# Performance work log

Measured on AMD Instinct MI355X. Metric: run time of the kernel, lower is better.

## Reference

```python
import jax, jax.numpy as jnp
import numpy as np

EPS = 1e-8
NUM_HEADS = 8
SCALE = 25.0
SIM_THRESH = 0.75
BLOCK = 10  # per-frame proposal group size used by the zeroing mask


def _l2norm(x):
    return x / (jnp.linalg.norm(x, axis=-1, keepdims=True) + EPS)


def setup_inputs() -> dict:
    key = jax.random.key(0)
    ks = jax.random.split(key, 7)
    B, N, C = 1, 2000, 256
    H = NUM_HEADS
    x_cls = jax.random.normal(ks[0], (B, N, C), dtype=jnp.float32)
    x_reg = jax.random.normal(ks[1], (B, N, C), dtype=jnp.float32)
    cls_score = jax.random.uniform(ks[2], (N,), dtype=jnp.float32)
    fg_score = jax.random.uniform(ks[3], (N,), dtype=jnp.float32)
    coord_attn = jax.random.uniform(ks[4], (B, H, N, N), dtype=jnp.float32)
    W_qkv_cls = jax.random.normal(ks[5], (3 * C, C), dtype=jnp.float32) * 0.02
    W_qkv_reg = jax.random.normal(ks[6], (3 * C, C), dtype=jnp.float32) * 0.02
    return {"x_cls": x_cls, "x_reg": x_reg, "cls_score": cls_score,
            "fg_score": fg_score, "coord_attn": coord_attn,
            "W_qkv_cls": W_qkv_cls, "W_qkv_reg": W_qkv_reg}


def reference(x_cls, x_reg, cls_score, fg_score, coord_attn, W_qkv_cls, W_qkv_reg):
    B, N, C = x_cls.shape
    H = NUM_HEADS
    D = C // H

    def qkv(x, W):
        t = (x @ W.T).reshape(B, N, 3, H, D).transpose(2, 0, 3, 1, 4)  # [3,B,H,N,D]
        return t[0], t[1], t[2]

    q_cls, k_cls, v_cls = qkv(x_cls, W_qkv_cls)
    q_reg, k_reg, v_reg = qkv(x_reg, W_qkv_reg)

    q_cls, k_cls = _l2norm(q_cls), _l2norm(k_cls)
    q_reg, k_reg = _l2norm(q_reg), _l2norm(k_reg)
    v_cls_normed = _l2norm(v_cls)

    cs = cls_score.reshape(1, 1, 1, N)  # broadcast over [B,H,N,N]
    fs = fg_score.reshape(1, 1, 1, N)

    attn_cls_raw = jnp.einsum('bhnd,bhmd->bhnm', v_cls_normed, v_cls_normed)

    attn_cls = jax.nn.softmax(jnp.einsum('bhnd,bhmd->bhnm', q_cls, k_cls) * SCALE * cs, axis=-1)
    attn_reg = jax.nn.softmax(jnp.einsum('bhnd,bhmd->bhnm', q_reg, k_reg) * SCALE * fs, axis=-1)

    attn = (attn_reg + attn_cls) * 0.5 * coord_attn
    attn = jax.lax.stop_gradient(attn)  # original detaches before masking

    # block-diagonal zeroing: row j zeros cols [j//10*10, j//10*10+9), keep diagonal
    rows = jnp.arange(N)[:, None]
    cols = jnp.arange(N)[None, :]
    block_start = (rows // BLOCK) * BLOCK
    zero_mask = (cols >= block_start) & (cols < block_start + (BLOCK - 1)) & (cols != rows)
    attn = jnp.where(zero_mask, 0.0, attn)

    x = jnp.einsum('bhnm,bhmd->bhnd', attn, v_cls).transpose(0, 2, 1, 3).reshape(B, N, C)
    x_ori = v_cls.transpose(0, 2, 1, 3).reshape(B, N, C)
    x_cat = jnp.concatenate([x, x_ori], axis=-1)  # [B,N,2C]

    # ave=True branch
    sim_raw = jnp.sum(attn_cls_raw, axis=1)[0] / H          # [N,N]
    sim_mask = (sim_raw > SIM_THRESH).astype(x_cls.dtype)
    sim_attn = jnp.sum(attn, axis=1)[0] / H                 # [N,N]
    sim_round2 = jax.nn.softmax(sim_attn, axis=-1)
    sim_round2 = sim_mask * sim_round2 / (jnp.sum(sim_mask * sim_round2, axis=-1, keepdims=True) + EPS)
    return x_cat, sim_round2
```

## Files before the change

### kernel.cpp

```cpp
#include <hip/hip_runtime.h>
#include <math.h>

typedef _Float16 half8 __attribute__((ext_vector_type(8)));
typedef _Float16 half4 __attribute__((ext_vector_type(4)));
typedef _Float16 half2v __attribute__((ext_vector_type(2)));
typedef float f32x4 __attribute__((ext_vector_type(4)));

constexpr int N = 2000;
constexpr int NP = 2048;
constexpr int H = 8;
constexpr int D = 32;
constexpr float SCL = 25.0f;
constexpr float L2E = 1.4426950408889634f;
constexpr float FM2 = 25.0f * L2E;

#define MFMA16(a,b,c)  __builtin_amdgcn_mfma_f32_16x16x32_f16((a),(b),(c),0,0,0)
#define MFMA16K(a,b,c) __builtin_amdgcn_mfma_f32_16x16x16f16((a),(b),(c),0,0,0)

__device__ __forceinline__ float fexp2(float x) { return __builtin_amdgcn_exp2f(x); }


__global__ __launch_bounds__(256) void wconv_kernel(
    const float* __restrict__ Wc, const float* __restrict__ Wr,
    _Float16* __restrict__ Wch, _Float16* __restrict__ Wrh)
{
    const int i = blockIdx.x * 256 + threadIdx.x;
    Wch[i] = (_Float16)Wc[i];
    Wrh[i] = (_Float16)Wr[i];
}

__global__ __launch_bounds__(256) void qkv_kernel(
    const float* __restrict__ xc, const float* __restrict__ xr,
    const _Float16* __restrict__ Wch, const _Float16* __restrict__ Wrh,
    const float* __restrict__ clsScore, const float* __restrict__ fgScore,
    _Float16* __restrict__ Qch, _Float16* __restrict__ Kch,
    _Float16* __restrict__ Qrh, _Float16* __restrict__ Krh,
    _Float16* __restrict__ Vnh, _Float16* __restrict__ Vth,
    float* __restrict__ out)
{
    constexpr int XS = 264;
    __shared__ _Float16 xs[16 * XS];
    const int t = threadIdx.x;
    const int n0 = blockIdx.x * 16;
    const int by = blockIdx.y;
    const int which = (by < 3) ? by : (by - 3);
    const bool isCls = by < 3;
    const float* x = isCls ? xc : xr;
    const _Float16* Wh = isCls ? Wch : Wrh;

    #pragma unroll
    for (int it = 0; it < 4; ++it) {
        const int f = t + it * 256;
        const int row = f >> 6, c4 = f & 63;
        const float4 v = *(const float4*)(x + (size_t)(n0 + row) * 256 + c4 * 4);
        half4 hv; hv[0]=(_Float16)v.x; hv[1]=(_Float16)v.y; hv[2]=(_Float16)v.z; hv[3]=(_Float16)v.w;
        *(half4*)&xs[row * XS + c4 * 4] = hv;
    }
    __syncthreads();

    const int w = t >> 6, l = t & 63;
    const int lr = l & 15, lg = l >> 4;
    const int obase = which * 256 + w * 64;
    f32x4 acc[4] = {{0,0,0,0},{0,0,0,0},{0,0,0,0},{0,0,0,0}};
    for (int k0 = 0; k0 < 256; k0 += 32) {
        const half8 aX = *(const half8*)&xs[lr * XS + k0 + lg * 8];
        #pragma unroll
        for (int s = 0; s < 4; ++s) {
            const half8 bW = *(const half8*)(Wh + (size_t)(obase + s * 16 + lr) * 256 + k0 + lg * 8);
            acc[s] = MFMA16(aX, bW, acc[s]);
        }
    }
    f32x4 kscale = {1.f,1.f,1.f,1.f};
    if (which == 1) {
        const float* sp = isCls ? clsScore : fgScore;
        kscale = (SCL * L2E) * *(const f32x4*)(sp + n0 + lg*4);
    }
    #pragma unroll
    for (int p = 0; p < 2; ++p) {
        const int h = 2 * w + p;
        float ss[4];
        #pragma unroll
        for (int j = 0; j < 4; ++j) {
            float v = acc[2*p][j]*acc[2*p][j] + acc[2*p+1][j]*acc[2*p+1][j];
            #pragma unroll
            for (int off = 1; off < 16; off <<= 1) v += __shfl_xor(v, off);
            ss[j] = sqrtf(v) + 1e-8f;
        }
        if (which < 2) {
            _Float16* Qd = isCls ? (which == 0 ? Qch : Kch) : (which == 0 ? Qrh : Krh);
            #pragma unroll
            for (int sh = 0; sh < 2; ++sh)
                #pragma unroll
                for (int j = 0; j < 4; ++j)
                    Qd[((size_t)h*NP + n0 + lg*4 + j)*D + sh*16 + lr]
                        = (_Float16)(acc[2*p+sh][j] / ss[j] * kscale[j]);
        } else {
            #pragma unroll
            for (int sh = 0; sh < 2; ++sh) {
                const int d = sh * 16 + lr;
                half4 tv;
                #pragma unroll
                for (int j = 0; j < 4; ++j) {
                    const float raw = acc[2*p+sh][j];
                    Vnh[((size_t)h*NP + n0 + lg*4 + j)*D + d] = (_Float16)(raw / ss[j]);
                    out[(size_t)(n0 + lg*4 + j)*512 + 256 + h*D + d] = raw;
                    tv[j] = (_Float16)raw;
                }
                *(half4*)(Vth + ((size_t)h*D + d)*NP + n0 + lg*4) = tv;
            }
        }
    }
}

__global__ __launch_bounds__(512) void stats_kernel(
    const _Float16* __restrict__ Qch, const _Float16* __restrict__ Kch,
    const _Float16* __restrict__ Qrh, const _Float16* __restrict__ Krh,
    float* __restrict__ BIAS)
{
    __shared__ float Ssh[4][2][16];
    const int t = threadIdx.x;
    const int w = t >> 6, l = t & 63;
    const int nsub = w >> 1, mhalf = w & 1;
    const int n0 = blockIdx.x * 64 + nsub * 16;
    const int h = blockIdx.y, z = blockIdx.z;
    const _Float16* Q = z ? Qrh : Qch;
    const _Float16* K = z ? Krh : Kch;
    const int lr = l & 15, lg = l >> 4;
    const half8 aQ = *(const half8*)(Q + ((size_t)h*NP + n0 + lr)*D + lg*8);
    float S[4] = {0.f, 0.f, 0.f, 0.f};
    const int msBeg = mhalf ? 63 : 0;
    const int msEnd = mhalf ? 125 : 63;
    half8 bK = *(const half8*)(K + ((size_t)h*NP + msBeg*16 + lr)*D + lg*8);
    for (int ms = msBeg; ms < msEnd; ++ms) {
        const half8 cur = bK;
        if (ms + 1 < msEnd)
            bK = *(const half8*)(K + ((size_t)h*NP + (ms+1)*16 + lr)*D + lg*8);
        f32x4 z4 = {0.f, 0.f, 0.f, 0.f};
        const f32x4 c = MFMA16(aQ, cur, z4);
        #pragma unroll
        for (int j = 0; j < 4; ++j) S[j] += fexp2(c[j] - FM2);
    }
    #pragma unroll
    for (int j = 0; j < 4; ++j) {
        #pragma unroll
        for (int off = 1; off < 16; off <<= 1) S[j] += __shfl_xor(S[j], off);
    }
    if (lr == 0) {
        #pragma unroll
        for (int j = 0; j < 4; ++j) Ssh[nsub][mhalf][lg*4 + j] = S[j];
    }
    __syncthreads();
    if (t < 64) {
        const int ns = t >> 4, rl = t & 15;
        BIAS[((size_t)z*H + h)*NP + blockIdx.x*64 + ns*16 + rl]
            = -__log2f(Ssh[ns][0][rl] + Ssh[ns][1][rl]) - FM2 - 1.0f;
    }
}

__global__ __launch_bounds__(256) void vvmask_kernel(
    const _Float16* __restrict__ Vnh, unsigned char* __restrict__ Mask)
{
    const int t = threadIdx.x;
    const int w = t >> 6, l = t & 63;
    const int n0 = blockIdx.y * 16;
    const int m00 = blockIdx.x * 256 + w * 64;
    const int lr = l & 15, lg = l >> 4;
    half8 aV[8];
    #pragma unroll
    for (int h = 0; h < 8; ++h)
        aV[h] = *(const half8*)(Vnh + ((size_t)(h*NP + n0 + lr))*D + lg*8);
    for (int s = 0; s < 4; ++s) {
        const int mb = m00 + s*16;
        f32x4 acc = {0.f, 0.f, 0.f, 0.f};
        #pragma unroll
        for (int h = 0; h < 8; ++h) {
            const half8 bV = *(const half8*)(Vnh + ((size_t)(h*NP + mb + lr))*D + lg*8);
            acc = MFMA16(aV[h], bV, acc);
        }
        const int m = mb + lr;
        if (m < N) {
            #pragma unroll
            for (int j = 0; j < 4; ++j) {
                const int n = n0 + lg*4 + j;
                Mask[(size_t)n*N + m] = (acc[j]*0.125f > 0.75f) ? (unsigned char)1 : (unsigned char)0;
            }
        }
    }
}

template<int SMAX>
__global__ __launch_bounds__(256, 4) void attn_kernel(
    const _Float16* __restrict__ Kch, const _Float16* __restrict__ Krh,
    const _Float16* __restrict__ Qch, const _Float16* __restrict__ Qrh,
    const _Float16* __restrict__ Vth, const float* __restrict__ coord,
    const float* __restrict__ BIAS,
    _Float16* __restrict__ SIMH, _Float16* __restrict__ XPH, int mcBase)
{
    __shared__ _Float16 simred[4][16][136];

    const int t = threadIdx.x;
    const int w = t >> 6, l = t & 63;
    const int lr = l & 15, lg = l >> 4;
    const int mc = mcBase + blockIdx.x;
    const int m0 = mc * 128;
    const int n0 = blockIdx.y * 16;
    const int n = n0 + lr;
    const int bs = (n / 10) * 10;
    const int h0 = 2 * w;

    unsigned kill = 0u;
    #pragma unroll
    for (int s = 0; s < SMAX; ++s)
        #pragma unroll
        for (int j = 0; j < 4; ++j) {
            const int m = m0 + s*16 + lg*4 + j;
            if (m >= bs && m < bs + 9 && m != n) kill |= (1u << (s*4 + j));
        }

    half8 aQc[2], aQr[2]; float bC[2], bR[2];
    #pragma unroll
    for (int p = 0; p < 2; ++p) {
        const int h = h0 + p;
        aQc[p] = *(const half8*)(Qch + ((size_t)h*NP + n)*D + lg*8);
        aQr[p] = *(const half8*)(Qrh + ((size_t)h*NP + n)*D + lg*8);
        bC[p] = BIAS[(size_t)h*NP + n];
        bR[p] = BIAS[(size_t)(H + h)*NP + n];
    }

    half2v sacc[SMAX][2];
    #pragma unroll
    for (int s = 0; s < SMAX; ++s)
        #pragma unroll
        for (int k = 0; k < 2; ++k) { sacc[s][k][0] = (_Float16)0.f; sacc[s][k][1] = (_Float16)0.f; }

    half8 kc[2], kr[2]; half4 v0[2], v1[2]; f32x4 co[2];
    auto LOAD = [&](int it) {
        const int p = it / SMAX, s = it % SMAX, b = it & 1;
        const int h = h0 + p;
        const size_t kb = ((size_t)h*NP + m0 + s*16 + lr)*D + lg*8;
        kc[b] = *(const half8*)(Kch + kb);
        kr[b] = *(const half8*)(Krh + kb);
        v0[b] = *(const half4*)(Vth + ((size_t)(h*D + lr))*NP + m0 + s*16 + lg*4);
        v1[b] = *(const half4*)(Vth + ((size_t)(h*D + 16 + lr))*NP + m0 + s*16 + lg*4);
        co[b] = *(const f32x4*)(coord + ((size_t)h*N + n)*N + m0 + s*16 + lg*4);
    };

    f32x4 pv0 = {0,0,0,0}, pv1 = {0,0,0,0};
    LOAD(0);
    #pragma unroll
    for (int it = 0; it < 2*SMAX; ++it) {
        const int p = it / SMAX, s = it % SMAX, b = it & 1;
        if (it + 1 < 2*SMAX) LOAD(it + 1);
        f32x4 z4 = {0.f,0.f,0.f,0.f};
        const f32x4 cc = MFMA16(kc[b], aQc[p], z4);
        const f32x4 cr = MFMA16(kr[b], aQr[p], z4);
        half4 af;
        #pragma unroll
        for (int j = 0; j < 4; ++j) {
            float a = (fexp2(cc[j] + bC[p]) + fexp2(cr[j] + bR[p])) * co[b][j];
            if ((kill >> (s*4 + j)) & 1u) a = 0.f;
            af[j] = (_Float16)a;
        }
        sacc[s][0] += (half2v){af[0], af[1]};
        sacc[s][1] += (half2v){af[2], af[3]};
        pv0 = MFMA16K(af, v0[b], pv0);
        pv1 = MFMA16K(af, v1[b], pv1);
        if (s == SMAX - 1) {
            const int h = h0 + p;
            _Float16* xp = XPH + (((size_t)(mc*H + h)*N + n0 + lg*4))*D + lr;
            #pragma unroll
            for (int j = 0; j < 4; ++j) {
                xp[j*D]      = (_Float16)pv0[j];
                xp[j*D + 16] = (_Float16)pv1[j];
            }
            pv0 = (f32x4){0,0,0,0}; pv1 = (f32x4){0,0,0,0};
        }
    }

    #pragma unroll
    for (int s = 0; s < SMAX; ++s) {
        half4 sv; sv[0]=sacc[s][0][0]; sv[1]=sacc[s][0][1]; sv[2]=sacc[s][1][0]; sv[3]=sacc[s][1][1];
        *(half4*)&simred[w][lr][s*16 + lg*4] = sv;
    }
    __syncthreads();
    constexpr int C8 = SMAX * 2;
    for (int e = t; e < 16 * C8; e += 256) {
        const int r = e / C8, c8 = e % C8;
        const half8 s0 = *(const half8*)&simred[0][r][c8*8];
        const half8 s1 = *(const half8*)&simred[1][r][c8*8];
        const half8 s2 = *(const half8*)&simred[2][r][c8*8];
        const half8 s3 = *(const half8*)&simred[3][r][c8*8];
        const half8 sum = (s0 + s1) + (s2 + s3);
        *(half8*)(SIMH + (size_t)(n0 + r)*N + m0 + c8*8) = sum;
    }
}

__global__ __launch_bounds__(256) void reduce_kernel(
    const _Float16* __restrict__ XPH, float* __restrict__ out)
{
    const int n = blockIdx.x, t = threadIdx.x;
    const int h = t >> 5, d = t & 31;
    float acc = 0.f;
    #pragma unroll
    for (int mcI = 0; mcI < 16; ++mcI)
        acc += (float)XPH[(((size_t)mcI*H + h)*N + n)*D + d];
    out[(size_t)n*512 + t] = acc;
}

__global__ __launch_bounds__(256) void simfinal_kernel(
    const _Float16* __restrict__ SIMH, const unsigned char* __restrict__ Mask,
    float* __restrict__ out)
{
    __shared__ float redA[4], redB[4];
    const int n = blockIdx.x, t = threadIdx.x;
    const _Float16* row = SIMH + (size_t)n * N;
    const unsigned char* mrow = Mask + (size_t)n * N;
    const bool act = t < 250;
    float f[8];
    unsigned int mk0 = 0, mk1 = 0;
    float mx = -1e30f;
    if (act) {
        const half8 v8 = *(const half8*)(row + t*8);
        const uint2 mm = *(const uint2*)(mrow + t*8);
        mk0 = mm.x; mk1 = mm.y;
        #pragma unroll
        for (int k = 0; k < 8; ++k) { f[k] = (float)v8[k]; mx = fmaxf(mx, f[k]); }
    }
    #pragma unroll
    for (int off = 1; off < 64; off <<= 1) mx = fmaxf(mx, __shfl_xor(mx, off));
    const int wv = t >> 6;
    if ((t & 63) == 0) redA[wv] = mx;
    __syncthreads();
    const float M = fmaxf(fmaxf(redA[0], redA[1]), fmaxf(redA[2], redA[3]));
    float e[8];
    float sA = 0.f, sM = 0.f;
    if (act) {
        #pragma unroll
        for (int k = 0; k < 8; ++k) {
            e[k] = fexp2((f[k] - M) * (L2E * 0.125f));
            sA += e[k];
            const unsigned int mkb = ((k < 4 ? mk0 : mk1) >> (8*(k & 3))) & 0xffu;
            if (mkb) sM += e[k]; else e[k] = 0.f;
        }
    }
    #pragma unroll
    for (int off = 1; off < 64; off <<= 1) { sA += __shfl_xor(sA, off); sM += __shfl_xor(sM, off); }
    __syncthreads();
    if ((t & 63) == 0) { redA[wv] = sA; redB[wv] = sM; }
    __syncthreads();
    const float SA = redA[0] + redA[1] + redA[2] + redA[3];
    const float SMK = redB[0] + redB[1] + redB[2] + redB[3];
    const float inv = 1.f / (SMK + 1e-8f * SA);
    if (act) {
        float* orow = out + 1024000 + (size_t)n*N + t*8;
        *(float4*)(orow)     = make_float4(e[0]*inv, e[1]*inv, e[2]*inv, e[3]*inv);
        *(float4*)(orow + 4) = make_float4(e[4]*inv, e[5]*inv, e[6]*inv, e[7]*inv);
    }
}

extern "C" void kernel_launch(void* const* d_in, const int* in_sizes, int n_in,
                              void* d_out, int out_size, void* d_ws, size_t ws_size,
                              hipStream_t stream) {
    const float* x_cls     = (const float*)d_in[0];
    const float* x_reg     = (const float*)d_in[1];
    const float* cls_score = (const float*)d_in[2];
    const float* fg_score  = (const float*)d_in[3];
    const float* coord     = (const float*)d_in[4];
    const float* Wc        = (const float*)d_in[5];
    const float* Wr        = (const float*)d_in[6];

    char* base = (char*)d_ws;
    float* BIAS     = (float*)base;
    _Float16* SIMH  = (_Float16*)(base + 131072);
    _Float16* XPH   = (_Float16*)(base + 8131072);
    _Float16* Qch   = (_Float16*)(base + 24515072);
    _Float16* Kch   = Qch + 524288;
    _Float16* Qrh   = Qch + 2*524288;
    _Float16* Krh   = Qch + 3*524288;
    _Float16* Vnh   = Qch + 4*524288;
    _Float16* Vth   = Qch + 5*524288;
    _Float16* Wch   = (_Float16*)(base + 30806528);
    _Float16* Wrh   = (_Float16*)(base + 31199744);
    unsigned char* Mask = (unsigned char*)(base + 31592960);
    float* out = (float*)d_out;

    wconv_kernel<<<768, 256, 0, stream>>>(Wc, Wr, Wch, Wrh);
    qkv_kernel<<<dim3(125, 5), 256, 0, stream>>>(x_cls, x_reg, Wch, Wrh, cls_score, fg_score,
                                                 Qch, Kch, Qrh, Krh, Vnh, Vth, out);
    stats_kernel<<<dim3(32, 8, 2), 512, 0, stream>>>(Qch, Kch, Qrh, Krh, BIAS);
    vvmask_kernel<<<dim3(8, 125), 256, 0, stream>>>(Vnh, Mask);
    attn_kernel<8><<<dim3(15, 125), 256, 0, stream>>>(Kch, Krh, Qch, Qrh, Vth, coord,
                                                      BIAS, SIMH, XPH, 0);
    attn_kernel<5><<<dim3(1, 125), 256, 0, stream>>>(Kch, Krh, Qch, Qrh, Vth, coord,
                                                     BIAS, SIMH, XPH, 15);
    reduce_kernel<<<2000, 256, 0, stream>>>(XPH, out);
    simfinal_kernel<<<2000, 256, 0, stream>>>(SIMH, Mask, out);
}
```

Baseline: 144.2 us.

## Deepen coord prefetch, raise attn occupancy, split stats key range four ways

The attention kernel now loads the coord_attn tile two iterations ahead using a three-slot buffer, separate from the one-ahead K/V prefetch, and its launch bounds ask for 5 blocks per SM instead of 4. The stats kernel now handles 32 query rows per block and splits the key range across four waves instead of two, giving 63 blocks per head instead of 32. The aim is to hide the latency of the large coord stream and to fill the GPU better in stats. The catch is more register pressure, which may cause spills under the tighter occupancy target.

```diff
diff --git a/kernel.cpp b/kernel.cpp
--- a/kernel.cpp
+++ b/kernel.cpp
@@ -117,23 +117,23 @@
     const _Float16* __restrict__ Qrh, const _Float16* __restrict__ Krh,
     float* __restrict__ BIAS)
 {
-    __shared__ float Ssh[4][2][16];
+    __shared__ float Ssh[2][4][16];
     const int t = threadIdx.x;
     const int w = t >> 6, l = t & 63;
-    const int nsub = w >> 1, mhalf = w & 1;
-    const int n0 = blockIdx.x * 64 + nsub * 16;
+    const int nsub = w >> 2, mq = w & 3;
+    const int n0 = blockIdx.x * 32 + nsub * 16;
     const int h = blockIdx.y, z = blockIdx.z;
     const _Float16* Q = z ? Qrh : Qch;
     const _Float16* K = z ? Krh : Kch;
     const int lr = l & 15, lg = l >> 4;
     const half8 aQ = *(const half8*)(Q + ((size_t)h*NP + n0 + lr)*D + lg*8);
     float S[4] = {0.f, 0.f, 0.f, 0.f};
-    const int msBeg = mhalf ? 63 : 0;
-    const int msEnd = mhalf ? 125 : 63;
-    half8 bK = *(const half8*)(K + ((size_t)h*NP + msBeg*16 + lr)*D + lg*8);
-    for (int ms = msBeg; ms < msEnd; ++ms) {
+    const int mqB0 = (mq == 0) ? 0 : 31*mq;
+    const int mqB1 = (mq == 3) ? 125 : 31*(mq+1);
+    half8 bK = *(const half8*)(K + ((size_t)h*NP + mqB0*16 + lr)*D + lg*8);
+    for (int ms = mqB0; ms < mqB1; ++ms) {
         const half8 cur = bK;
-        if (ms + 1 < msEnd)
+        if (ms + 1 < mqB1)
             bK = *(const half8*)(K + ((size_t)h*NP + (ms+1)*16 + lr)*D + lg*8);
         f32x4 z4 = {0.f, 0.f, 0.f, 0.f};
         const f32x4 c = MFMA16(aQ, cur, z4);
@@ -147,13 +147,14 @@
     }
     if (lr == 0) {
         #pragma unroll
-        for (int j = 0; j < 4; ++j) Ssh[nsub][mhalf][lg*4 + j] = S[j];
-    }
-    __syncthreads();
-    if (t < 64) {
+        for (int j = 0; j < 4; ++j) Ssh[nsub][mq][lg*4 + j] = S[j];
+    }
+    __syncthreads();
+    if (t < 32) {
         const int ns = t >> 4, rl = t & 15;
-        BIAS[((size_t)z*H + h)*NP + blockIdx.x*64 + ns*16 + rl]
-            = -__log2f(Ssh[ns][0][rl] + Ssh[ns][1][rl]) - FM2 - 1.0f;
+        const int n = blockIdx.x * 32 + ns*16 + rl;
+        BIAS[((size_t)z*H + h)*NP + n]
+            = -__log2f(Ssh[ns][0][rl] + Ssh[ns][1][rl] + Ssh[ns][2][rl] + Ssh[ns][3][rl]) - FM2 - 1.0f;
     }
 }
 
@@ -189,7 +190,7 @@
 }
 
 template<int SMAX>
-__global__ __launch_bounds__(256, 4) void attn_kernel(
+__global__ __launch_bounds__(256, 5) void attn_kernel(
     const _Float16* __restrict__ Kch, const _Float16* __restrict__ Krh,
     const _Float16* __restrict__ Qch, const _Float16* __restrict__ Qrh,
     const _Float16* __restrict__ Vth, const float* __restrict__ coord,
@@ -233,8 +234,13 @@
         #pragma unroll
         for (int k = 0; k < 2; ++k) { sacc[s][k][0] = (_Float16)0.f; sacc[s][k][1] = (_Float16)0.f; }
 
-    half8 kc[2], kr[2]; half4 v0[2], v1[2]; f32x4 co[2];
-    auto LOAD = [&](int it) {
+    half8 kc[2], kr[2]; half4 v0[2], v1[2]; f32x4 co[3];
+    auto LOADCO = [&](int it) {
+        const int p = it / SMAX, s = it % SMAX, c = it % 3;
+        const int h = h0 + p;
+        co[c] = *(const f32x4*)(coord + ((size_t)h*N + n)*N + m0 + s*16 + lg*4);
+    };
+    auto LOADKV = [&](int it) {
         const int p = it / SMAX, s = it % SMAX, b = it & 1;
         const int h = h0 + p;
         const size_t kb = ((size_t)h*NP + m0 + s*16 + lr)*D + lg*8;
@@ -242,22 +248,24 @@
         kr[b] = *(const half8*)(Krh + kb);
         v0[b] = *(const half4*)(Vth + ((size_t)(h*D + lr))*NP + m0 + s*16 + lg*4);
         v1[b] = *(const half4*)(Vth + ((size_t)(h*D + 16 + lr))*NP + m0 + s*16 + lg*4);
-        co[b] = *(const f32x4*)(coord + ((size_t)h*N + n)*N + m0 + s*16 + lg*4);
     };
 
     f32x4 pv0 = {0,0,0,0}, pv1 = {0,0,0,0};
-    LOAD(0);
+    LOADCO(0);
+    if (2*SMAX > 1) LOADCO(1);
+    LOADKV(0);
     #pragma unroll
     for (int it = 0; it < 2*SMAX; ++it) {
-        const int p = it / SMAX, s = it % SMAX, b = it & 1;
-        if (it + 1 < 2*SMAX) LOAD(it + 1);
+        const int p = it / SMAX, s = it % SMAX, b = it & 1, c = it % 3;
+        if (it + 2 < 2*SMAX) LOADCO(it + 2);
+        if (it + 1 < 2*SMAX) LOADKV(it + 1);
         f32x4 z4 = {0.f,0.f,0.f,0.f};
         const f32x4 cc = MFMA16(kc[b], aQc[p], z4);
         const f32x4 cr = MFMA16(kr[b], aQr[p], z4);
         half4 af;
         #pragma unroll
         for (int j = 0; j < 4; ++j) {
-            float a = (fexp2(cc[j] + bC[p]) + fexp2(cr[j] + bR[p])) * co[b][j];
+            float a = (fexp2(cc[j] + bC[p]) + fexp2(cr[j] + bR[p])) * co[c][j];
             if ((kill >> (s*4 + j)) & 1u) a = 0.f;
             af[j] = (_Float16)a;
         }
@@ -387,7 +395,7 @@
     wconv_kernel<<<768, 256, 0, stream>>>(Wc, Wr, Wch, Wrh);
     qkv_kernel<<<dim3(125, 5), 256, 0, stream>>>(x_cls, x_reg, Wch, Wrh, cls_score, fg_score,
                                                  Qch, Kch, Qrh, Krh, Vnh, Vth, out);
-    stats_kernel<<<dim3(32, 8, 2), 512, 0, stream>>>(Qch, Kch, Qrh, Krh, BIAS);
+    stats_kernel<<<dim3(63, 8, 2), 512, 0, stream>>>(Qch, Kch, Qrh, Krh, BIAS);
     vvmask_kernel<<<dim3(8, 125), 256, 0, stream>>>(Vnh, Mask);
     attn_kernel<8><<<dim3(15, 125), 256, 0, stream>>>(Kch, Krh, Qch, Qrh, Vth, coord,
                                                       BIAS, SIMH, XPH, 0);
```

New measurement: 136.2 us. 5.6% less time.
